# Performance work log

Hardware: AMD Instinct MI355X
Metric: run time of the kernel (lower is better)

The kernel has to match this reference:

```python
import jax, jax.numpy as jnp
import numpy as np

BATCH, NODE, DIM = 4, 2048, 128
EPS = 1e-5


def _bn(x, gamma, beta):
    # BatchNorm1d in training mode: biased batch stats over rows, per-feature.
    mu = jnp.mean(x, axis=0)
    var = jnp.var(x, axis=0)
    return (x - mu) * jax.lax.rsqrt(var + EPS) * gamma + beta


def setup_inputs() -> dict:
    key = jax.random.key(0)
    ks = jax.random.split(key, 8)
    N = BATCH * NODE
    # Scale L like a normalized graph operator so activations stay sane.
    L = jax.random.normal(ks[0], (N, N), dtype=jnp.float32) / np.sqrt(N)
    inputs = jax.random.normal(ks[1], (BATCH, NODE, DIM), dtype=jnp.float32)
    mask = jnp.zeros((BATCH, NODE, 1), dtype=bool)  # unused in forward
    lim = 1.0 / np.sqrt(2 * DIM)
    fc0_w = jax.random.uniform(ks[2], (DIM, 2 * DIM), jnp.float32, -lim, lim)
    fc0_b = jax.random.uniform(ks[3], (DIM,), jnp.float32, -lim, lim)
    fc1_w = jax.random.uniform(ks[4], (DIM, 2 * DIM), jnp.float32, -lim, lim)
    fc1_b = jax.random.uniform(ks[5], (DIM,), jnp.float32, -lim, lim)
    bn0_gamma = jnp.ones((2 * DIM,), jnp.float32)
    bn0_beta = jnp.zeros((2 * DIM,), jnp.float32)
    bn1_gamma = jnp.ones((2 * DIM,), jnp.float32)
    bn1_beta = jnp.zeros((2 * DIM,), jnp.float32)
    return dict(L=L, mask=mask, inputs=inputs,
                bn0_gamma=bn0_gamma, bn0_beta=bn0_beta, fc0_w=fc0_w, fc0_b=fc0_b,
                bn1_gamma=bn1_gamma, bn1_beta=bn1_beta, fc1_w=fc1_w, fc1_b=fc1_b)


def reference(L, mask, inputs, bn0_gamma, bn0_beta, fc0_w, fc0_b,
              bn1_gamma, bn1_beta, fc1_w, fc1_b):
    b, n, d = inputs.shape

    def block(x, gamma, beta, w, bias):
        # x: (b, n, d). Laplacian propagation over flattened batch*node dim.
        xf = x.reshape(-1, d)                      # (b*n, d)
        Lx = (L @ xf).reshape(b, n, d)
        h = jnp.concatenate([x, Lx], axis=2).reshape(-1, 2 * d)
        h = _bn(h, gamma, beta)                    # pre-BN
        h = h @ w.T + bias                         # Linear(2d -> d)
        return h.reshape(b, n, d)

    x = jax.nn.elu(inputs)
    x = block(x, bn0_gamma, bn0_beta, fc0_w, fc0_b)
    x = jax.nn.elu(x)
    x = block(x, bn1_gamma, bn1_beta, fc1_w, fc1_b)
    return x + inputs
```

## Files before the change

### kernel.cpp

```cpp
#include <hip/hip_runtime.h>
#include <math.h>

#define NROWS 8192
#define DIM   128
#define FEAT  256
#define BK    128
#define NT    (NROWS / BK)

typedef __attribute__((ext_vector_type(8))) __bf16 bf16x8;
typedef __attribute__((ext_vector_type(8))) unsigned short u16x8;
typedef __attribute__((ext_vector_type(4))) unsigned short u16x4;
typedef __attribute__((ext_vector_type(4))) float f32x4;

__device__ __forceinline__ float bf2f(unsigned short h) {
  return __uint_as_float(((unsigned)h) << 16);
}
__device__ __forceinline__ unsigned short f2bf(float f) {
  unsigned u = __float_as_uint(f);
  return (unsigned short)((u + 0x7fff + ((u >> 16) & 1)) >> 16);
}
__device__ __forceinline__ void async16(const void* g, void* l) {
  __builtin_amdgcn_global_load_lds(
      (const __attribute__((address_space(1))) void*)g,
      (__attribute__((address_space(3))) void*)l, 16, 0, 0);
}
__device__ __forceinline__ f32x4 mfma16(bf16x8 a, bf16x8 b, f32x4 c) {
  return __builtin_amdgcn_mfma_f32_16x16x32_bf16(a, b, c, 0, 0, 0);
}
__device__ __forceinline__ float ldp(const void* p, int i, int is32) {
  return is32 ? ((const float*)p)[i] : bf2f(((const unsigned short*)p)[i]);
}

__global__ void detect_kernel(const unsigned short* __restrict__ L,
                              int* __restrict__ flag,
                              float* __restrict__ stats)
{
  for (int i = threadIdx.x; i < 1024; i += 256) stats[i] = 0.f;
  __shared__ int cnt;
  if (threadIdx.x == 0) cnt = 0;
  __syncthreads();
  int c = 0;
  for (int i = 0; i < 16; i++) {
    unsigned short s = L[2 * (threadIdx.x + 256 * i)];
    int e = (s >> 7) & 0xFF;
    if (e >= 192) c++;
  }
  atomicAdd(&cnt, c);
  __syncthreads();
  if (threadIdx.x == 0) *flag = (cnt > 16) ? 1 : 0;
}

__global__ __launch_bounds__(256) void trans_kernel(
    const void* __restrict__ src, unsigned short* __restrict__ xT,
    unsigned short* __restrict__ x0, unsigned short* __restrict__ inpc,
    float* __restrict__ stats, const int* __restrict__ flag)
{
  __shared__ __align__(16) unsigned short T[128 * 136];
  const int tid = threadIdx.x;
  const int r0 = blockIdx.x * 128;
  const int is32 = *flag;
  #pragma unroll
  for (int i = 0; i < 8; i++) {
    const int c = tid + 256 * i;
    const int rr = c >> 4, cg = c & 15;
    const size_t gidx = (size_t)(r0 + rr) * DIM + cg * 8;
    u16x8 v;
    if (is32) {
      const float* s = (const float*)src + gidx;
      f32x4 a = *(const f32x4*)s, b = *(const f32x4*)(s + 4);
      #pragma unroll
      for (int e = 0; e < 4; e++) { v[e] = f2bf(a[e]); v[e + 4] = f2bf(b[e]); }
    } else {
      v = *(const u16x8*)((const unsigned short*)src + gidx);
    }
    *(u16x8*)(inpc + gidx) = v;
    #pragma unroll
    for (int e = 0; e < 8; e++) {
      float f = bf2f(v[e]);
      f = f > 0.f ? f : expm1f(f);
      v[e] = f2bf(f);
    }
    *(u16x8*)(x0 + gidx) = v;
    *(u16x8*)(T + rr * 136 + cg * 8) = v;
  }
  __syncthreads();
  #pragma unroll
  for (int i = 0; i < 8; i++) {
    const int c = tid + 256 * i;
    const int n = c >> 4, mg = c & 15;
    u16x8 v;
    float s = 0.f, q = 0.f;
    #pragma unroll
    for (int e = 0; e < 8; e++) {
      unsigned short h = T[(mg * 8 + e) * 136 + n];
      v[e] = h;
      float f = bf2f(h);
      s += f; q += f * f;
    }
    *(u16x8*)(xT + (size_t)n * NROWS + r0 + mg * 8) = v;
    #pragma unroll
    for (int off = 1; off < 16; off <<= 1) {
      s += __shfl_xor(s, off, 16);
      q += __shfl_xor(q, off, 16);
    }
    if ((tid & 15) == 0) {
      atomicAdd(&stats[n], s);
      atomicAdd(&stats[256 + n], q);
    }
  }
}

template <int IS32>
__device__ __forceinline__ void gemm1_body(
    const void* __restrict__ Lraw, const unsigned short* __restrict__ xT,
    unsigned short* __restrict__ Lxb, float* __restrict__ stats,
    unsigned short* __restrict__ AsBase, unsigned short* __restrict__ BsBase)
{
  const int tid  = threadIdx.x;
  const int lane = tid & 63;
  const int wave = tid >> 6;
  const int kh = wave >> 2, wq = wave & 3;
  const int ln = lane & 15, quad = lane >> 4;
  const int m0 = blockIdx.x * 32;

  const int arow = tid >> 4, ap = tid & 15;
  const int akg = (ap & 8) | ((ap & 7) ^ (arow & 7));
  const float*          Lf = (const float*)Lraw;
  const unsigned short* Lh = (const unsigned short*)Lraw;
  const size_t Abase = (size_t)(m0 + arow) * NROWS + akg * 8;

  int brow[4], bkg[4];
  #pragma unroll
  for (int i = 0; i < 4; i++) {
    const int c = tid + (i << 9);
    brow[i] = c >> 4;
    const int p = c & 15;
    bkg[i] = (p & 8) | ((p & 7) ^ (brow[i] & 7));
  }

  unsigned short* a0 = AsBase;
  unsigned short* a1 = AsBase + 32 * 128;
  unsigned short* a2 = AsBase + 2 * 32 * 128;
  unsigned short* c0 = BsBase;
  unsigned short* c1 = BsBase + 128 * 128;
  unsigned short* c2 = BsBase + 2 * 128 * 128;

  f32x4 acc[2][2];
  #pragma unroll
  for (int i = 0; i < 2; i++)
    #pragma unroll
    for (int j = 0; j < 2; j++)
      acc[i][j] = (f32x4){0.f, 0.f, 0.f, 0.f};

  auto issueB = [&](int kt, unsigned short* Bbuf) {
    const size_t koff = (size_t)kt * BK;
    #pragma unroll
    for (int i = 0; i < 4; i++) {
      const int c = tid + (i << 9);
      async16(xT + (size_t)brow[i] * NROWS + koff + bkg[i] * 8, Bbuf + c * 8);
    }
  };
  auto loadA = [&](int kt, f32x4& r0, f32x4& r1) {
    const float* s = Lf + Abase + (size_t)kt * BK;
    r0 = *(const f32x4*)s;
    r1 = *(const f32x4*)(s + 4);
  };
  auto issueA16 = [&](int kt, unsigned short* Abuf) {
    async16(Lh + Abase + (size_t)kt * BK, Abuf + arow * 128 + ap * 8);
  };
  auto writeA = [&](const f32x4& r0, const f32x4& r1, unsigned short* Abuf) {
    u16x8 o;
    #pragma unroll
    for (int e = 0; e < 4; e++) { o[e] = f2bf(r0[e]); o[e + 4] = f2bf(r1[e]); }
    *(u16x8*)(Abuf + arow * 128 + ap * 8) = o;
  };
  auto compute = [&](const unsigned short* Abuf, const unsigned short* Bbuf) {
    #pragma unroll
    for (int s = 0; s < 2; s++) {
      const int kga = kh * 8 + s * 4 + quad;
      const int sw8 = ((kga & 8) | ((kga & 7) ^ (ln & 7))) * 8;
      bf16x8 af0 = *(const bf16x8*)(Abuf + ln * 128 + sw8);
      bf16x8 af1 = *(const bf16x8*)(Abuf + (16 + ln) * 128 + sw8);
      bf16x8 bf0 = *(const bf16x8*)(Bbuf + (wq * 32 + ln) * 128 + sw8);
      bf16x8 bf1 = *(const bf16x8*)(Bbuf + (wq * 32 + 16 + ln) * 128 + sw8);
      acc[0][0] = mfma16(af0, bf0, acc[0][0]);
      acc[0][1] = mfma16(af0, bf1, acc[0][1]);
      acc[1][0] = mfma16(af1, bf0, acc[1][0]);
      acc[1][1] = mfma16(af1, bf1, acc[1][1]);
    }
  };
  auto waitbar = [&]() {
    if (IS32) asm volatile("s_waitcnt vmcnt(6) lgkmcnt(0)" ::: "memory");
    else      asm volatile("s_waitcnt vmcnt(5) lgkmcnt(0)" ::: "memory");
    __builtin_amdgcn_s_barrier();
  };

  f32x4 e0, e1, o0, o1;

  issueB(0, c0);
  if (IS32) loadA(0, e0, e1); else issueA16(0, a0);
  issueB(1, c1);
  if (IS32) loadA(1, o0, o1); else issueA16(1, a1);
  if (IS32) writeA(e0, e1, a0);
  waitbar();

  for (int p = 0; p < 31; ++p) {
    const int t = 2 * p;
    issueB(t + 2, c2);
    if (IS32) loadA(t + 2, e0, e1); else issueA16(t + 2, a2);
    compute(a0, c0);
    if (IS32) writeA(o0, o1, a1);
    waitbar();
    issueB(t + 3, c0);
    if (IS32) loadA(t + 3, o0, o1); else issueA16(t + 3, a0);
    compute(a1, c1);
    if (IS32) writeA(e0, e1, a2);
    waitbar();
    unsigned short* tB = c2; c2 = c1; c1 = c0; c0 = tB;
    unsigned short* tA = a2; a2 = a1; a1 = a0; a0 = tA;
  }

  compute(a0, c0);
  if (IS32) writeA(o0, o1, a1);
  __syncthreads();
  compute(a1, c1);
  __syncthreads();

  float* E = (float*)AsBase;
  if (kh == 0) {
    #pragma unroll
    for (int i = 0; i < 2; i++)
      #pragma unroll
      for (int j = 0; j < 2; j++)
        #pragma unroll
        for (int r = 0; r < 4; r++)
          E[(i * 16 + quad * 4 + r) * 128 + wq * 32 + j * 16 + ln] =
              acc[i][j][r];
  }
  __syncthreads();
  if (kh == 1) {
    #pragma unroll
    for (int i = 0; i < 2; i++)
      #pragma unroll
      for (int j = 0; j < 2; j++)
        #pragma unroll
        for (int r = 0; r < 4; r++)
          E[(i * 16 + quad * 4 + r) * 128 + wq * 32 + j * 16 + ln] +=
              acc[i][j][r];
  }
  __syncthreads();
  {
    const int row = tid >> 4, cc0 = (tid & 15) * 8;
    u16x8 o;
    #pragma unroll
    for (int e = 0; e < 8; e++) o[e] = f2bf(E[row * 128 + cc0 + e]);
    *(u16x8*)(Lxb + (size_t)(m0 + row) * DIM + cc0) = o;
  }
  if (tid < 128) {
    float s = 0.f, q = 0.f;
    #pragma unroll
    for (int r = 0; r < 32; r++) {
      const float v = E[r * 128 + tid];
      s += v; q += v * v;
    }
    atomicAdd(&stats[128 + tid], s);
    atomicAdd(&stats[384 + tid], q);
  }
}

__global__ __launch_bounds__(512) void gemm1_fused(
    const void* __restrict__ Lraw, const unsigned short* __restrict__ xT,
    unsigned short* __restrict__ Lxb, float* __restrict__ stats,
    const int* __restrict__ flag)
{
  __shared__ __align__(16) unsigned short As[3 * 32 * 128];
  __shared__ __align__(16) unsigned short Bs[3 * 128 * 128];
  if (*flag) gemm1_body<1>(Lraw, xT, Lxb, stats, As, Bs);
  else       gemm1_body<0>(Lraw, xT, Lxb, stats, As, Bs);
}

__global__ void prep_kernel(const float* __restrict__ stats,
                            const void* __restrict__ gamma,
                            const void* __restrict__ beta,
                            const void* __restrict__ w,
                            const void* __restrict__ bias,
                            unsigned short* __restrict__ weff,
                            float* __restrict__ beff,
                            const int* __restrict__ flag)
{
  const int is32 = *flag;
  const int k = blockIdx.x;
  const int j = threadIdx.x;
  const float inv = 1.f / 8192.f;
  float mu = stats[j] * inv;
  float var = fmaxf(stats[256 + j] * inv - mu * mu, 0.f);
  float s = ldp(gamma, j, is32) * rsqrtf(var + 1e-5f);
  float wv = ldp(w, k * FEAT + j, is32);
  weff[(size_t)k * FEAT + j] = f2bf(wv * s);
  float term = (ldp(beta, j, is32) - mu * s) * wv;
  __shared__ float red[256];
  red[j] = term;
  __syncthreads();
  for (int off = 128; off > 0; off >>= 1) {
    if (j < off) red[j] += red[j + off];
    __syncthreads();
  }
  if (j == 0) beff[k] = ldp(bias, k, is32) + red[0];
}

__global__ __launch_bounds__(256) void gemm2_fc(
    const unsigned short* __restrict__ xb,
    const unsigned short* __restrict__ Lxb,
    const unsigned short* __restrict__ weff,
    const float* __restrict__ beff,
    const unsigned short* __restrict__ resid,
    void* __restrict__ outv,
    unsigned short* __restrict__ xTout,
    float* __restrict__ statsOut,
    int mode, const int* __restrict__ flag)
{
  __shared__ __align__(16) unsigned short As[32 * 264];
  const int is32 = *flag;
  const int tid = threadIdx.x;
  const int lane = tid & 63, wave = tid >> 6;
  const int m0 = blockIdx.x * 32;

  #pragma unroll
  for (int i = 0; i < 4; i++) {
    const int c = tid + 256 * i;
    const int mr = c >> 5, ch = c & 31;
    const unsigned short* src =
        (ch < 16) ? (xb  + (size_t)(m0 + mr) * DIM + ch * 8)
                  : (Lxb + (size_t)(m0 + mr) * DIM + (ch - 16) * 8);
    *(u16x8*)(As + mr * 264 + ch * 8) = *(const u16x8*)src;
  }
  __syncthreads();

  const int ln = lane & 15, quad = lane >> 4;
  const int nq = wave * 32;
  f32x4 acc[2][2];
  #pragma unroll
  for (int i = 0; i < 2; i++)
    #pragma unroll
    for (int j = 0; j < 2; j++)
      acc[i][j] = (f32x4){0.f, 0.f, 0.f, 0.f};

  #pragma unroll
  for (int ks = 0; ks < 8; ks++) {
    bf16x8 af[2], bfr[2];
    #pragma unroll
    for (int i = 0; i < 2; i++)
      af[i] = *(const bf16x8*)(As + (i * 16 + ln) * 264 + ks * 32 + quad * 8);
    #pragma unroll
    for (int j = 0; j < 2; j++)
      bfr[j] = *(const bf16x8*)(weff + (size_t)(nq + j * 16 + ln) * FEAT +
                                ks * 32 + quad * 8);
    #pragma unroll
    for (int i = 0; i < 2; i++)
      #pragma unroll
      for (int j = 0; j < 2; j++)
        acc[i][j] = mfma16(af[i], bfr[j], acc[i][j]);
  }

  #pragma unroll
  for (int j = 0; j < 2; j++) {
    const int gn = nq + j * 16 + ln;
    const float bb = beff[gn];
    float s = 0.f, q = 0.f;
    #pragma unroll
    for (int i = 0; i < 2; i++) {
      u16x4 pk;
      #pragma unroll
      for (int r = 0; r < 4; r++) {
        const int gm = m0 + i * 16 + quad * 4 + r;
        float v = acc[i][j][r] + bb;
        const size_t idx = (size_t)gm * DIM + gn;
        if (mode == 0) {
          v = v > 0.f ? v : expm1f(v);
          const unsigned short h = f2bf(v);
          ((unsigned short*)outv)[idx] = h;
          pk[r] = h;
          const float hv = bf2f(h);
          s += hv; q += hv * hv;
        } else {
          v += bf2f(resid[idx]);
          if (is32) ((float*)outv)[idx] = v;
          else      ((unsigned short*)outv)[idx] = f2bf(v);
        }
      }
      if (mode == 0)
        *(u16x4*)(xTout + (size_t)gn * NROWS + m0 + i * 16 + quad * 4) = pk;
    }
    if (mode == 0) {
      s += __shfl_xor(s, 16); q += __shfl_xor(q, 16);
      s += __shfl_xor(s, 32); q += __shfl_xor(q, 32);
      if (quad == 0) {
        atomicAdd(&statsOut[gn], s);
        atomicAdd(&statsOut[256 + gn], q);
      }
    }
  }
}

extern "C" void kernel_launch(void* const* d_in, const int* in_sizes, int n_in,
                              void* d_out, int out_size, void* d_ws, size_t ws_size,
                              hipStream_t stream) {
  const void* Lm   = d_in[0];
  const void* inp  = d_in[2];
  const void* bn0g = d_in[3];
  const void* bn0b = d_in[4];
  const void* fc0w = d_in[5];
  const void* fc0b = d_in[6];
  const void* bn1g = d_in[7];
  const void* bn1b = d_in[8];
  const void* fc1w = d_in[9];
  const void* fc1b = d_in[10];

  char* ws = (char*)d_ws;
  unsigned short* xT   = (unsigned short*)(ws);
  unsigned short* x0   = (unsigned short*)(ws + (2ull << 20));
  unsigned short* Lxb  = (unsigned short*)(ws + (4ull << 20));
  unsigned short* x1   = (unsigned short*)(ws + (6ull << 20));
  unsigned short* inpc = (unsigned short*)(ws + (8ull << 20));
  float*          stats= (float*)         (ws + (10ull << 20));
  int*            flag = (int*)           (ws + (10ull << 20) + 8192);
  float*          beff = (float*)         (ws + (10ull << 20) + 12288);
  unsigned short* weff = (unsigned short*)(ws + (10ull << 20) + 16384);

  detect_kernel<<<1, 256, 0, stream>>>((const unsigned short*)Lm, flag, stats);

  trans_kernel<<<64, 256, 0, stream>>>(inp, xT, x0, inpc, stats, flag);
  gemm1_fused<<<256, 512, 0, stream>>>(Lm, xT, Lxb, stats, flag);
  prep_kernel<<<128, 256, 0, stream>>>(stats, bn0g, bn0b, fc0w, fc0b,
                                       weff, beff, flag);
  gemm2_fc<<<256, 256, 0, stream>>>(x0, Lxb, weff, beff, nullptr, x1,
                                    xT, stats + 512, 0, flag);

  gemm1_fused<<<256, 512, 0, stream>>>(Lm, xT, Lxb, stats + 512, flag);
  prep_kernel<<<128, 256, 0, stream>>>(stats + 512, bn1g, bn1b, fc1w, fc1b,
                                       weff, beff, flag);
  gemm2_fc<<<256, 256, 0, stream>>>(x1, Lxb, weff, beff, inpc, d_out,
                                    nullptr, nullptr, 1, flag);
}
```

Measured before the change: 180.0 us.

## Split the Laplacian GEMM over K with a separate reduce-and-stats kernel

The L@x GEMM now splits K into two halves across a second grid dimension, which doubles the number of blocks from 256 to 512 and fills more compute units. The K tile shrinks to 64 so each block uses less LDS. Each half writes fp32 partials to a workspace buffer, and a new lx_reduce kernel sums them, converts the result to bf16 and accumulates the batchnorm stats. The bf16 A path now loads through registers instead of async LDS loads. The cost is an extra kernel launch and an extra round trip through memory for fp32 partials of about 8 MB per block.

```diff
diff --git a/kernel.cpp b/kernel.cpp
--- a/kernel.cpp
+++ b/kernel.cpp
@@ -4,8 +4,10 @@
 #define NROWS 8192
 #define DIM   128
 #define FEAT  256
-#define BK    128
-#define NT    (NROWS / BK)
+#define BKS   64
+#define KSPL  2
+#define KCH   (NROWS / KSPL)
+#define NTS   (KCH / BKS)
 
 typedef __attribute__((ext_vector_type(8))) __bf16 bf16x8;
 typedef __attribute__((ext_vector_type(8))) unsigned short u16x8;
@@ -113,7 +115,7 @@
 template <int IS32>
 __device__ __forceinline__ void gemm1_body(
     const void* __restrict__ Lraw, const unsigned short* __restrict__ xT,
-    unsigned short* __restrict__ Lxb, float* __restrict__ stats,
+    float* __restrict__ Lxp,
     unsigned short* __restrict__ AsBase, unsigned short* __restrict__ BsBase)
 {
   const int tid  = threadIdx.x;
@@ -122,28 +124,32 @@
   const int kh = wave >> 2, wq = wave & 3;
   const int ln = lane & 15, quad = lane >> 4;
   const int m0 = blockIdx.x * 32;
-
-  const int arow = tid >> 4, ap = tid & 15;
-  const int akg = (ap & 8) | ((ap & 7) ^ (arow & 7));
+  const int koff0 = blockIdx.y * KCH;
+
+  const int arow = tid >> 4, as = tid & 15;
+  const int ac = as >> 1, ah = as & 1;
+  const int ap = ac ^ (arow & 7);
+  const int aLds = arow * 64 + ap * 8 + ah * 4;
+  const int aGk = ac * 8 + ah * 4;
   const float*          Lf = (const float*)Lraw;
   const unsigned short* Lh = (const unsigned short*)Lraw;
-  const size_t Abase = (size_t)(m0 + arow) * NROWS + akg * 8;
-
-  int brow[4], bkg[4];
-  #pragma unroll
-  for (int i = 0; i < 4; i++) {
+  const size_t Abase = (size_t)(m0 + arow) * NROWS + koff0 + aGk;
+
+  int brow[2], bkg[2];
+  #pragma unroll
+  for (int i = 0; i < 2; i++) {
     const int c = tid + (i << 9);
-    brow[i] = c >> 4;
-    const int p = c & 15;
-    bkg[i] = (p & 8) | ((p & 7) ^ (brow[i] & 7));
+    brow[i] = c >> 3;
+    const int p = c & 7;
+    bkg[i] = p ^ (brow[i] & 7);
   }
 
   unsigned short* a0 = AsBase;
-  unsigned short* a1 = AsBase + 32 * 128;
-  unsigned short* a2 = AsBase + 2 * 32 * 128;
+  unsigned short* a1 = AsBase + 32 * 64;
+  unsigned short* a2 = AsBase + 2 * 32 * 64;
   unsigned short* c0 = BsBase;
-  unsigned short* c1 = BsBase + 128 * 128;
-  unsigned short* c2 = BsBase + 2 * 128 * 128;
+  unsigned short* c1 = BsBase + 128 * 64;
+  unsigned short* c2 = BsBase + 2 * 128 * 64;
 
   f32x4 acc[2][2];
   #pragma unroll
@@ -153,80 +159,78 @@
       acc[i][j] = (f32x4){0.f, 0.f, 0.f, 0.f};
 
   auto issueB = [&](int kt, unsigned short* Bbuf) {
-    const size_t koff = (size_t)kt * BK;
-    #pragma unroll
-    for (int i = 0; i < 4; i++) {
+    const size_t koff = (size_t)koff0 + kt * BKS;
+    #pragma unroll
+    for (int i = 0; i < 2; i++) {
       const int c = tid + (i << 9);
       async16(xT + (size_t)brow[i] * NROWS + koff + bkg[i] * 8, Bbuf + c * 8);
     }
   };
-  auto loadA = [&](int kt, f32x4& r0, f32x4& r1) {
-    const float* s = Lf + Abase + (size_t)kt * BK;
-    r0 = *(const f32x4*)s;
-    r1 = *(const f32x4*)(s + 4);
-  };
-  auto issueA16 = [&](int kt, unsigned short* Abuf) {
-    async16(Lh + Abase + (size_t)kt * BK, Abuf + arow * 128 + ap * 8);
-  };
-  auto writeA = [&](const f32x4& r0, const f32x4& r1, unsigned short* Abuf) {
-    u16x8 o;
-    #pragma unroll
-    for (int e = 0; e < 4; e++) { o[e] = f2bf(r0[e]); o[e + 4] = f2bf(r1[e]); }
-    *(u16x8*)(Abuf + arow * 128 + ap * 8) = o;
+  auto loadA32 = [&](int kt, f32x4& r) {
+    r = *(const f32x4*)(Lf + Abase + (size_t)kt * BKS);
+  };
+  auto loadA16 = [&](int kt, u16x4& r) {
+    r = *(const u16x4*)(Lh + Abase + (size_t)kt * BKS);
+  };
+  auto writeA32 = [&](const f32x4& r, unsigned short* Abuf) {
+    u16x4 o;
+    #pragma unroll
+    for (int e = 0; e < 4; e++) o[e] = f2bf(r[e]);
+    *(u16x4*)(Abuf + aLds) = o;
+  };
+  auto writeA16 = [&](const u16x4& r, unsigned short* Abuf) {
+    *(u16x4*)(Abuf + aLds) = r;
   };
   auto compute = [&](const unsigned short* Abuf, const unsigned short* Bbuf) {
-    #pragma unroll
-    for (int s = 0; s < 2; s++) {
-      const int kga = kh * 8 + s * 4 + quad;
-      const int sw8 = ((kga & 8) | ((kga & 7) ^ (ln & 7))) * 8;
-      bf16x8 af0 = *(const bf16x8*)(Abuf + ln * 128 + sw8);
-      bf16x8 af1 = *(const bf16x8*)(Abuf + (16 + ln) * 128 + sw8);
-      bf16x8 bf0 = *(const bf16x8*)(Bbuf + (wq * 32 + ln) * 128 + sw8);
-      bf16x8 bf1 = *(const bf16x8*)(Bbuf + (wq * 32 + 16 + ln) * 128 + sw8);
-      acc[0][0] = mfma16(af0, bf0, acc[0][0]);
-      acc[0][1] = mfma16(af0, bf1, acc[0][1]);
-      acc[1][0] = mfma16(af1, bf0, acc[1][0]);
-      acc[1][1] = mfma16(af1, bf1, acc[1][1]);
-    }
+    const int kga = kh * 4 + quad;
+    const int sw8 = (kga ^ (ln & 7)) * 8;
+    bf16x8 af0 = *(const bf16x8*)(Abuf + ln * 64 + sw8);
+    bf16x8 af1 = *(const bf16x8*)(Abuf + (16 + ln) * 64 + sw8);
+    bf16x8 bf0 = *(const bf16x8*)(Bbuf + (wq * 32 + ln) * 64 + sw8);
+    bf16x8 bf1 = *(const bf16x8*)(Bbuf + (wq * 32 + 16 + ln) * 64 + sw8);
+    acc[0][0] = mfma16(af0, bf0, acc[0][0]);
+    acc[0][1] = mfma16(af0, bf1, acc[0][1]);
+    acc[1][0] = mfma16(af1, bf0, acc[1][0]);
+    acc[1][1] = mfma16(af1, bf1, acc[1][1]);
   };
   auto waitbar = [&]() {
-    if (IS32) asm volatile("s_waitcnt vmcnt(6) lgkmcnt(0)" ::: "memory");
-    else      asm volatile("s_waitcnt vmcnt(5) lgkmcnt(0)" ::: "memory");
+    asm volatile("s_waitcnt vmcnt(3) lgkmcnt(0)" ::: "memory");
     __builtin_amdgcn_s_barrier();
   };
 
-  f32x4 e0, e1, o0, o1;
+  f32x4 e32, o32;
+  u16x4 e16, o16;
 
   issueB(0, c0);
-  if (IS32) loadA(0, e0, e1); else issueA16(0, a0);
+  if (IS32) loadA32(0, e32); else loadA16(0, e16);
   issueB(1, c1);
-  if (IS32) loadA(1, o0, o1); else issueA16(1, a1);
-  if (IS32) writeA(e0, e1, a0);
+  if (IS32) loadA32(1, o32); else loadA16(1, o16);
+  if (IS32) writeA32(e32, a0); else writeA16(e16, a0);
   waitbar();
 
   for (int p = 0; p < 31; ++p) {
     const int t = 2 * p;
     issueB(t + 2, c2);
-    if (IS32) loadA(t + 2, e0, e1); else issueA16(t + 2, a2);
+    if (IS32) loadA32(t + 2, e32); else loadA16(t + 2, e16);
     compute(a0, c0);
-    if (IS32) writeA(o0, o1, a1);
+    if (IS32) writeA32(o32, a1); else writeA16(o16, a1);
     waitbar();
     issueB(t + 3, c0);
-    if (IS32) loadA(t + 3, o0, o1); else issueA16(t + 3, a0);
+    if (IS32) loadA32(t + 3, o32); else loadA16(t + 3, o16);
     compute(a1, c1);
-    if (IS32) writeA(e0, e1, a2);
+    if (IS32) writeA32(e32, a2); else writeA16(e16, a2);
     waitbar();
     unsigned short* tB = c2; c2 = c1; c1 = c0; c0 = tB;
     unsigned short* tA = a2; a2 = a1; a1 = a0; a0 = tA;
   }
 
   compute(a0, c0);
-  if (IS32) writeA(o0, o1, a1);
+  if (IS32) writeA32(o32, a1); else writeA16(o16, a1);
   __syncthreads();
   compute(a1, c1);
   __syncthreads();
 
-  float* E = (float*)AsBase;
+  float* E = (float*)BsBase;
   if (kh == 0) {
     #pragma unroll
     for (int i = 0; i < 2; i++)
@@ -250,33 +254,40 @@
   }
   __syncthreads();
   {
+    float* dst = Lxp + (size_t)blockIdx.y * (NROWS * DIM);
     const int row = tid >> 4, cc0 = (tid & 15) * 8;
-    u16x8 o;
-    #pragma unroll
-    for (int e = 0; e < 8; e++) o[e] = f2bf(E[row * 128 + cc0 + e]);
-    *(u16x8*)(Lxb + (size_t)(m0 + row) * DIM + cc0) = o;
-  }
-  if (tid < 128) {
-    float s = 0.f, q = 0.f;
-    #pragma unroll
-    for (int r = 0; r < 32; r++) {
-      const float v = E[r * 128 + tid];
-      s += v; q += v * v;
-    }
-    atomicAdd(&stats[128 + tid], s);
-    atomicAdd(&stats[384 + tid], q);
-  }
-}
-
-__global__ __launch_bounds__(512) void gemm1_fused(
+    *(f32x4*)(dst + (size_t)(m0 + row) * DIM + cc0) =
+        *(const f32x4*)(E + row * 128 + cc0);
+    *(f32x4*)(dst + (size_t)(m0 + row) * DIM + cc0 + 4) =
+        *(const f32x4*)(E + row * 128 + cc0 + 4);
+  }
+}
+
+__global__ __launch_bounds__(512) void gemm1_splitk(
     const void* __restrict__ Lraw, const unsigned short* __restrict__ xT,
-    unsigned short* __restrict__ Lxb, float* __restrict__ stats,
-    const int* __restrict__ flag)
-{
-  __shared__ __align__(16) unsigned short As[3 * 32 * 128];
-  __shared__ __align__(16) unsigned short Bs[3 * 128 * 128];
-  if (*flag) gemm1_body<1>(Lraw, xT, Lxb, stats, As, Bs);
-  else       gemm1_body<0>(Lraw, xT, Lxb, stats, As, Bs);
+    float* __restrict__ Lxp, const int* __restrict__ flag)
+{
+  __shared__ __align__(16) unsigned short As[3 * 32 * 64];
+  __shared__ __align__(16) unsigned short Bs[3 * 128 * 64];
+  if (*flag) gemm1_body<1>(Lraw, xT, Lxp, As, Bs);
+  else       gemm1_body<0>(Lraw, xT, Lxp, As, Bs);
+}
+
+__global__ void lx_reduce(const float* __restrict__ Lxp,
+                          unsigned short* __restrict__ Lxb,
+                          float* __restrict__ stats)
+{
+  const int col = threadIdx.x;
+  const int r0 = blockIdx.x * 32;
+  float s = 0.f, q = 0.f;
+  for (int i = 0; i < 32; i++) {
+    const size_t base = (size_t)(r0 + i) * DIM + col;
+    float v = Lxp[base] + Lxp[(size_t)(NROWS * DIM) + base];
+    Lxb[base] = f2bf(v);
+    s += v; q += v * v;
+  }
+  atomicAdd(&stats[128 + col], s);
+  atomicAdd(&stats[384 + col], q);
 }
 
 __global__ void prep_kernel(const float* __restrict__ stats,
@@ -426,17 +437,20 @@
   int*            flag = (int*)           (ws + (10ull << 20) + 8192);
   float*          beff = (float*)         (ws + (10ull << 20) + 12288);
   unsigned short* weff = (unsigned short*)(ws + (10ull << 20) + 16384);
+  float*          Lxp  = (float*)         (ws + (12ull << 20));
 
   detect_kernel<<<1, 256, 0, stream>>>((const unsigned short*)Lm, flag, stats);
 
   trans_kernel<<<64, 256, 0, stream>>>(inp, xT, x0, inpc, stats, flag);
-  gemm1_fused<<<256, 512, 0, stream>>>(Lm, xT, Lxb, stats, flag);
+  gemm1_splitk<<<dim3(256, KSPL), 512, 0, stream>>>(Lm, xT, Lxp, flag);
+  lx_reduce<<<256, 128, 0, stream>>>(Lxp, Lxb, stats);
   prep_kernel<<<128, 256, 0, stream>>>(stats, bn0g, bn0b, fc0w, fc0b,
                                        weff, beff, flag);
   gemm2_fc<<<256, 256, 0, stream>>>(x0, Lxb, weff, beff, nullptr, x1,
                                     xT, stats + 512, 0, flag);
 
-  gemm1_fused<<<256, 512, 0, stream>>>(Lm, xT, Lxb, stats + 512, flag);
+  gemm1_splitk<<<dim3(256, KSPL), 512, 0, stream>>>(Lm, xT, Lxp, flag);
+  lx_reduce<<<256, 128, 0, stream>>>(Lxp, Lxb, stats + 512);
   prep_kernel<<<128, 256, 0, stream>>>(stats + 512, bn1g, bn1b, fc1w, fc1b,
                                        weff, beff, flag);
   gemm2_fc<<<256, 256, 0, stream>>>(x1, Lxb, weff, beff, inpc, d_out,
```

New measurement: 196.2 us. +9.0%, slower.
